# Performance work log

Measured on AMD Instinct MI355X. Metric: run time of the kernel, lower is better.

## Reference

```python
import jax, jax.numpy as jnp
import numpy as np

B, D, M = 32, 640, 1024
EPS = 1e-05


def setup_inputs() -> dict:
    key = jax.random.key(0)
    x = jax.random.normal(key, (B, D, M), dtype=jnp.float32)
    return {"x": x}


def _triu_flat_indices(d):
    iu, ju = np.triu_indices(d)
    return jnp.asarray(iu * d + ju, dtype=jnp.int32)


def reference(x):
    b, d, m = x.shape
    # Gram matrix: x @ x^T  -> [b, d, d]
    x_pow2 = jnp.einsum('bim,bjm->bij', x, x)
    # I_M @ (x_pow2 * I) + (x_pow2 * I) @ I_M - 2*x_pow2
    # (x_pow2 * I) is diagonal, so ones-matrix bmm = broadcast of the diagonal.
    diag = jnp.diagonal(x_pow2, axis1=1, axis2=2)  # [b, d]
    dcov = diag[:, None, :] + diag[:, :, None] - 2.0 * x_pow2
    dcov = jnp.maximum(dcov, 0.0)
    # temperature param is built in-forward: exp(log(1/(2*d*m))) = 1/(2*d*m)
    temperature = 1.0 / (2.0 * d * m)
    dcov = jnp.sqrt(temperature * dcov + EPS)
    # Double centering: dcov @ I_M = row sums broadcast; I_M @ dcov = col sums.
    row_mean = dcov.sum(axis=2, keepdims=True) / d          # [b, d, 1]
    col_mean = dcov.sum(axis=1, keepdims=True) / d          # [b, 1, d]
    tot_mean = dcov.sum(axis=(1, 2), keepdims=True) / (d * d)
    t = dcov - row_mean - col_mean + tot_mean               # [b, d, d]
    # Triuvec: gather upper-triangular entries (incl. diagonal)
    flat_idx = _triu_flat_indices(d)                         # [d*(d+1)//2]
    y = t.reshape(b, d * d)[:, flat_idx]
    return y
```

## Files before the change

### kernel.cpp

```cpp
#include <hip/hip_runtime.h>

#define D_DIM 640
#define M_DIM 1024
#define B_DIM 32
#define BK 32
#define OUT_ROW 205120

typedef __bf16 bf16x8 __attribute__((ext_vector_type(8)));
typedef float f32x4 __attribute__((ext_vector_type(4)));

__device__ __forceinline__ unsigned short f2bf(float f) {
    union { float f; unsigned int u; } c; c.f = f;
    unsigned int u = c.u;
    unsigned int r = (u + 0x7fffu + ((u >> 16) & 1u)) >> 16;
    return (unsigned short)r;
}

__device__ __forceinline__ void gload_lds16(const unsigned short* g, unsigned short* l) {
    __builtin_amdgcn_global_load_lds(
        (const __attribute__((address_space(1))) unsigned int*)g,
        (__attribute__((address_space(3))) unsigned int*)l,
        16, 0, 0);
}

__device__ __forceinline__ float block_reduce_256(float s) {
    #pragma unroll
    for (int off = 32; off > 0; off >>= 1) s += __shfl_down(s, off, 64);
    __shared__ float red[4];
    if ((threadIdx.x & 63) == 0) red[threadIdx.x >> 6] = s;
    __syncthreads();
    return red[0] + red[1] + red[2] + red[3];
}

__global__ void cast_diag_kernel(const float* __restrict__ x,
                                 unsigned short* __restrict__ xb,
                                 float* __restrict__ diag,
                                 float* __restrict__ rowsum,
                                 float* __restrict__ tot) {
    const size_t row = blockIdx.x;
    const int t = threadIdx.x;
    const float4 v = ((const float4*)(x + row * M_DIM))[t];
    float s = v.x * v.x + v.y * v.y + v.z * v.z + v.w * v.w;
    ushort4 o;
    o.x = f2bf(v.x); o.y = f2bf(v.y); o.z = f2bf(v.z); o.w = f2bf(v.w);
    ((ushort4*)(xb + row * M_DIM))[t] = o;
    float ssum = block_reduce_256(s);
    if (t == 0) { diag[row] = ssum; rowsum[row] = 0.f; }
    if (t == 1 && row < B_DIM) tot[row] = 0.f;
}

__global__ __launch_bounds__(256, 2)
void gemm_dcov_kernel(const unsigned short* __restrict__ xb,
                      const float* __restrict__ diag,
                      float* __restrict__ dcov,
                      float* __restrict__ rowsum,
                      float* __restrict__ tot) {
    __shared__ __align__(16) unsigned short smem[24576];

    const int id = blockIdx.x;
    const int bt = (id & 7) * 4 + ((id >> 3) & 3);
    int p = id >> 5;
    int it = 0, off = p;
    while (off >= 5 - it) { off -= 5 - it; ++it; }
    const int jt = it + off;
    const bool diagTile = (it == jt);

    const int tid = threadIdx.x;
    const int w = tid >> 6, l = tid & 63;
    const int wy = w >> 1, wx = w & 1;
    const int lm = l & 15, quad = l >> 4;

    const unsigned short* gA = xb + ((size_t)bt * D_DIM + it * 128) * M_DIM;
    const unsigned short* gB = xb + ((size_t)bt * D_DIM + jt * 128) * M_DIM;

    const int r0 = tid >> 2;
    const int cl = (((tid & 3) ^ ((tid >> 3) & 3)) << 3);
    const size_t aoff1 = (size_t)r0 * M_DIM + cl;
    const size_t aoff2 = aoff1 + (size_t)64 * M_DIM;
    const int ldst = tid * 8;

    auto issue = [&](int k, int ph) {
        unsigned short* sA = smem + ph * 8192;
        unsigned short* sB = sA + 4096;
        const int koff = k * BK;
        gload_lds16(gA + aoff1 + koff, sA + ldst);
        gload_lds16(gA + aoff2 + koff, sA + ldst + 2048);
        gload_lds16(gB + aoff1 + koff, sB + ldst);
        gload_lds16(gB + aoff2 + koff, sB + ldst + 2048);
    };

    f32x4 acc[4][4];
    const f32x4 zero = {0.f, 0.f, 0.f, 0.f};
    #pragma unroll
    for (int i = 0; i < 4; i++)
        #pragma unroll
        for (int j = 0; j < 4; j++) acc[i][j] = zero;

    const int sw = ((quad ^ ((lm >> 1) & 3)) << 3);

    issue(0, 0); issue(1, 1); issue(2, 2);

    int ph = 0;
    for (int k = 0; k < 32; ++k) {
        if (k < 30)       asm volatile("s_waitcnt vmcnt(8)" ::: "memory");
        else if (k == 30) asm volatile("s_waitcnt vmcnt(4)" ::: "memory");
        else              asm volatile("s_waitcnt vmcnt(0)" ::: "memory");
        asm volatile("s_barrier" ::: "memory");

        const unsigned short* sA = smem + ph * 8192;
        const unsigned short* sB = sA + 4096;
        bf16x8 af[4], bfr[4];
        #pragma unroll
        for (int mi = 0; mi < 4; mi++)
            af[mi] = *(const bf16x8*)&sA[(wy * 64 + mi * 16 + lm) * BK + sw];
        #pragma unroll
        for (int ni = 0; ni < 4; ni++)
            bfr[ni] = *(const bf16x8*)&sB[(wx * 64 + ni * 16 + lm) * BK + sw];

        #pragma unroll
        for (int mi = 0; mi < 4; mi++)
            #pragma unroll
            for (int ni = 0; ni < 4; ni++)
                acc[mi][ni] = __builtin_amdgcn_mfma_f32_16x16x32_bf16(
                    af[mi], bfr[ni], acc[mi][ni], 0, 0, 0);

        asm volatile("s_barrier" ::: "memory");
        if (k + 3 < 32) issue(k + 3, ph);
        ph = (ph == 2) ? 0 : ph + 1;
    }

    float* sd = (float*)smem;
    if (tid < 128) sd[tid] = diag[(size_t)bt * D_DIM + it * 128 + tid];
    else           sd[tid] = diag[(size_t)bt * D_DIM + jt * 128 + (tid - 128)];
    __syncthreads();

    const float temp = 7.62939453125e-07f;
    float* dbase = dcov + (size_t)bt * D_DIM * D_DIM;
    float* rs = rowsum + (size_t)bt * D_DIM;
    float ts = 0.f;
    float cp[4] = {0.f, 0.f, 0.f, 0.f};

    #pragma unroll
    for (int mi = 0; mi < 4; mi++) {
        #pragma unroll
        for (int r = 0; r < 4; r++) {
            const int lrow = wy * 64 + mi * 16 + quad * 4 + r;
            const int grow = it * 128 + lrow;
            const float di = sd[lrow];
            float rp = 0.f;
            #pragma unroll
            for (int ni = 0; ni < 4; ni++) {
                const int lcol = wx * 64 + ni * 16 + lm;
                const int gcol = jt * 128 + lcol;
                const float dj = sd[128 + lcol];
                const float g = acc[mi][ni][r];
                const float v = sqrtf(fmaf(temp, fmaxf(di + dj - 2.f * g, 0.f), 1e-5f));
                dbase[(size_t)grow * D_DIM + gcol] = v;
                rp += v;
                cp[ni] += v;
            }
            ts += rp;
            rp += __shfl_down(rp, 8, 16);
            rp += __shfl_down(rp, 4, 16);
            rp += __shfl_down(rp, 2, 16);
            rp += __shfl_down(rp, 1, 16);
            if (lm == 0) atomicAdd(&rs[grow], rp);
        }
    }
    if (!diagTile) {
        #pragma unroll
        for (int ni = 0; ni < 4; ni++) {
            float c = cp[ni];
            c += __shfl_down(c, 32);
            c += __shfl_down(c, 16);
            if (l < 16) atomicAdd(&rs[jt * 128 + wx * 64 + ni * 16 + lm], c);
        }
    }
    float bs = block_reduce_256(ts);
    if (tid == 0) atomicAdd(&tot[bt], diagTile ? bs : 2.f * bs);
}

__global__ void output_kernel(const float* __restrict__ dcov,
                              const float* __restrict__ rowsum,
                              const float* __restrict__ tot,
                              float* __restrict__ out) {
    const int b = blockIdx.x / D_DIM;
    const int i = blockIdx.x - b * D_DIM;
    const float inv_d = 1.f / (float)D_DIM;
    const float rmi = rowsum[(size_t)b * D_DIM + i] * inv_d;
    const float tm = tot[b] * (inv_d * inv_d);
    const float* drow = dcov + ((size_t)b * D_DIM + i) * D_DIM;
    const float* rs = rowsum + (size_t)b * D_DIM;
    float* orow = out + (size_t)b * OUT_ROW + (size_t)i * D_DIM - (size_t)i * (i - 1) / 2;
    for (int j = i + threadIdx.x; j < D_DIM; j += 256)
        orow[j - i] = drow[j] - rmi - rs[j] * inv_d + tm;
}

extern "C" void kernel_launch(void* const* d_in, const int* in_sizes, int n_in,
                              void* d_out, int out_size, void* d_ws, size_t ws_size,
                              hipStream_t stream) {
    const float* x = (const float*)d_in[0];
    float* out = (float*)d_out;

    char* ws = (char*)d_ws;
    unsigned short* xb = (unsigned short*)ws;
    size_t off = 41943040;
    float* diag = (float*)(ws + off);   off += 81920;
    float* dcov = (float*)(ws + off);   off += 52428800;
    float* rowsum = (float*)(ws + off); off += 81920;
    float* tot = (float*)(ws + off);    off += 256;

    cast_diag_kernel<<<dim3(B_DIM * D_DIM), 256, 0, stream>>>(x, xb, diag, rowsum, tot);
    gemm_dcov_kernel<<<dim3(480), 256, 0, stream>>>(xb, diag, dcov, rowsum, tot);
    output_kernel<<<dim3(B_DIM * D_DIM), 256, 0, stream>>>(dcov, rowsum, tot, out);
}
```

Before: 175.7 us.

## Fuse output centering into GEMM via grid-wide barrier, drop dcov buffer

Removes the intermediate dcov matrix and the separate output kernel. After each GEMM block accumulates its row and total sums, all blocks meet at a global atomic-counter barrier, then recompute the distances from the accumulators still held in registers and write the centered upper-triangular output directly. This avoids writing and re-reading about 52 MB of dcov and saves one kernel launch. The cost is a spin barrier that relies on all 480 blocks being resident at once (2 per CU on 256 CUs), plus the sqrt work being done a second time.

```diff
diff --git a/kernel.cpp b/kernel.cpp
--- a/kernel.cpp
+++ b/kernel.cpp
@@ -5,6 +5,7 @@
 #define B_DIM 32
 #define BK 32
 #define OUT_ROW 205120
+#define NBLK 480
 
 typedef __bf16 bf16x8 __attribute__((ext_vector_type(8)));
 typedef float f32x4 __attribute__((ext_vector_type(4)));
@@ -32,11 +33,16 @@
     return red[0] + red[1] + red[2] + red[3];
 }
 
+__device__ __forceinline__ float aload(const float* p) {
+    return __hip_atomic_load(p, __ATOMIC_RELAXED, __HIP_MEMORY_SCOPE_AGENT);
+}
+
 __global__ void cast_diag_kernel(const float* __restrict__ x,
                                  unsigned short* __restrict__ xb,
                                  float* __restrict__ diag,
                                  float* __restrict__ rowsum,
-                                 float* __restrict__ tot) {
+                                 float* __restrict__ tot,
+                                 unsigned int* __restrict__ ctr) {
     const size_t row = blockIdx.x;
     const int t = threadIdx.x;
     const float4 v = ((const float4*)(x + row * M_DIM))[t];
@@ -47,14 +53,17 @@
     float ssum = block_reduce_256(s);
     if (t == 0) { diag[row] = ssum; rowsum[row] = 0.f; }
     if (t == 1 && row < B_DIM) tot[row] = 0.f;
+    if (t == 2 && row == 0)
+        __hip_atomic_store(ctr, 0u, __ATOMIC_RELAXED, __HIP_MEMORY_SCOPE_AGENT);
 }
 
 __global__ __launch_bounds__(256, 2)
-void gemm_dcov_kernel(const unsigned short* __restrict__ xb,
-                      const float* __restrict__ diag,
-                      float* __restrict__ dcov,
-                      float* __restrict__ rowsum,
-                      float* __restrict__ tot) {
+void gemm_out_kernel(const unsigned short* __restrict__ xb,
+                     const float* __restrict__ diag,
+                     float* __restrict__ rowsum,
+                     float* __restrict__ tot,
+                     unsigned int* __restrict__ ctr,
+                     float* __restrict__ out) {
     __shared__ __align__(16) unsigned short smem[24576];
 
     const int id = blockIdx.x;
@@ -135,7 +144,6 @@
     __syncthreads();
 
     const float temp = 7.62939453125e-07f;
-    float* dbase = dcov + (size_t)bt * D_DIM * D_DIM;
     float* rs = rowsum + (size_t)bt * D_DIM;
     float ts = 0.f;
     float cp[4] = {0.f, 0.f, 0.f, 0.f};
@@ -151,11 +159,9 @@
             #pragma unroll
             for (int ni = 0; ni < 4; ni++) {
                 const int lcol = wx * 64 + ni * 16 + lm;
-                const int gcol = jt * 128 + lcol;
                 const float dj = sd[128 + lcol];
                 const float g = acc[mi][ni][r];
                 const float v = sqrtf(fmaf(temp, fmaxf(di + dj - 2.f * g, 0.f), 1e-5f));
-                dbase[(size_t)grow * D_DIM + gcol] = v;
                 rp += v;
                 cp[ni] += v;
             }
@@ -178,22 +184,44 @@
     }
     float bs = block_reduce_256(ts);
     if (tid == 0) atomicAdd(&tot[bt], diagTile ? bs : 2.f * bs);
-}
-
-__global__ void output_kernel(const float* __restrict__ dcov,
-                              const float* __restrict__ rowsum,
-                              const float* __restrict__ tot,
-                              float* __restrict__ out) {
-    const int b = blockIdx.x / D_DIM;
-    const int i = blockIdx.x - b * D_DIM;
+
+    __threadfence();
+    __syncthreads();
+    if (tid == 0) {
+        atomicAdd(ctr, 1u);
+        while (__hip_atomic_load(ctr, __ATOMIC_ACQUIRE, __HIP_MEMORY_SCOPE_AGENT) < NBLK)
+            __builtin_amdgcn_s_sleep(2);
+    }
+    __syncthreads();
+
     const float inv_d = 1.f / (float)D_DIM;
-    const float rmi = rowsum[(size_t)b * D_DIM + i] * inv_d;
-    const float tm = tot[b] * (inv_d * inv_d);
-    const float* drow = dcov + ((size_t)b * D_DIM + i) * D_DIM;
-    const float* rs = rowsum + (size_t)b * D_DIM;
-    float* orow = out + (size_t)b * OUT_ROW + (size_t)i * D_DIM - (size_t)i * (i - 1) / 2;
-    for (int j = i + threadIdx.x; j < D_DIM; j += 256)
-        orow[j - i] = drow[j] - rmi - rs[j] * inv_d + tm;
+    const float tm = aload(&tot[bt]) * (inv_d * inv_d);
+    float cmj[4];
+    #pragma unroll
+    for (int ni = 0; ni < 4; ni++)
+        cmj[ni] = aload(&rs[jt * 128 + wx * 64 + ni * 16 + lm]) * inv_d;
+
+    float* obase = out + (size_t)bt * OUT_ROW;
+    #pragma unroll
+    for (int mi = 0; mi < 4; mi++) {
+        #pragma unroll
+        for (int r = 0; r < 4; r++) {
+            const int lrow = wy * 64 + mi * 16 + quad * 4 + r;
+            const int grow = it * 128 + lrow;
+            const float di = sd[lrow];
+            const float rmi = aload(&rs[grow]) * inv_d;
+            float* orow = obase + (size_t)grow * D_DIM - (size_t)grow * (grow - 1) / 2 - grow;
+            #pragma unroll
+            for (int ni = 0; ni < 4; ni++) {
+                const int gcol = jt * 128 + wx * 64 + ni * 16 + lm;
+                const float dj = sd[128 + (wx * 64 + ni * 16 + lm)];
+                const float g = acc[mi][ni][r];
+                const float v = sqrtf(fmaf(temp, fmaxf(di + dj - 2.f * g, 0.f), 1e-5f));
+                if (!diagTile || gcol >= grow)
+                    orow[gcol] = v - rmi - cmj[ni] + tm;
+            }
+        }
+    }
 }
 
 extern "C" void kernel_launch(void* const* d_in, const int* in_sizes, int n_in,
@@ -205,12 +233,11 @@
     char* ws = (char*)d_ws;
     unsigned short* xb = (unsigned short*)ws;
     size_t off = 41943040;
-    float* diag = (float*)(ws + off);   off += 81920;
-    float* dcov = (float*)(ws + off);   off += 52428800;
-    float* rowsum = (float*)(ws + off); off += 81920;
-    float* tot = (float*)(ws + off);    off += 256;
-
-    cast_diag_kernel<<<dim3(B_DIM * D_DIM), 256, 0, stream>>>(x, xb, diag, rowsum, tot);
-    gemm_dcov_kernel<<<dim3(480), 256, 0, stream>>>(xb, diag, dcov, rowsum, tot);
-    output_kernel<<<dim3(B_DIM * D_DIM), 256, 0, stream>>>(dcov, rowsum, tot, out);
-}
+    float* diag = (float*)(ws + off);     off += 81920;
+    float* rowsum = (float*)(ws + off);   off += 81920;
+    float* tot = (float*)(ws + off);      off += 256;
+    unsigned int* ctr = (unsigned int*)(ws + off); off += 256;
+
+    cast_diag_kernel<<<dim3(B_DIM * D_DIM), 256, 0, stream>>>(x, xb, diag, rowsum, tot, ctr);
+    gemm_out_kernel<<<dim3(NBLK), 256, 0, stream>>>(xb, diag, rowsum, tot, ctr, out);
+}
```

Measured after the change: 221.7 us. 26.2% more time.
